# Kernel optimization log

Measured on AMD Instinct MI355X. Metric: run time of the kernel, lower is better.

## Reference

```python
import jax, jax.numpy as jnp
import numpy as np

EPS = 1.1920929e-07  # torch F.rms_norm default eps for fp32
D, NH, NKV, HD = 1024, 16, 4, 64
MLP_MULT, L = 3, 6           # L = num_layers // 2 shared blocks
VS, HS, LS, ROPE_B = 50257, 4096, 30.0, 10000.0
B, S = 2, 2048


def rmsn(x):
    return x * jax.lax.rsqrt(jnp.mean(jnp.square(x), -1, keepdims=True) + EPS)


def rope_tables(s):
    f = 1.0 / ROPE_B ** (jnp.arange(0, HD, 2, dtype=jnp.float32) / HD)
    fr = jnp.outer(jnp.arange(s, dtype=jnp.float32), f)  # [s, HD/2]
    return jnp.cos(fr), jnp.sin(fr)


def rot(x, c, s):
    h = x.shape[-1] // 2
    x1, x2 = x[..., :h], x[..., h:]
    return jnp.concatenate([x1 * c + x2 * s, -x1 * s + x2 * c], -1)


def attn(x, Wq, Wk, Wv, Wo, qg, cos, sin):
    b, s, d = x.shape
    q = (x @ Wq.T).reshape(b, s, NH, HD).swapaxes(1, 2)    # [b,nh,s,hd]
    k = (x @ Wk.T).reshape(b, s, NKV, HD).swapaxes(1, 2)   # [b,nkv,s,hd]
    v = (x @ Wv.T).reshape(b, s, NKV, HD).swapaxes(1, 2)
    q, k = rmsn(q), rmsn(k)                                # QK RMSNorm (no weight)
    c, si = cos[None, None], sin[None, None]
    q, k = rot(q, c, si), rot(k, c, si)
    q = q * qg[None, :, None, None]                        # per-head gate
    g = NH // NKV
    qr = q.reshape(b, NKV, g, s, HD)
    scores = jnp.einsum('bkgqd,bksd->bkgqs', qr, k) / jnp.sqrt(jnp.float32(HD))
    mask = jnp.tril(jnp.ones((s, s), bool))
    scores = jnp.where(mask, scores, -jnp.inf)
    p = jax.nn.softmax(scores, -1)
    y = jnp.einsum('bkgqs,bksd->bkgqd', p, v).reshape(b, NH, s, HD)
    y = y.swapaxes(1, 2).reshape(b, s, d)
    return y @ Wo.T


def mlp(x, Wf, Wo2):
    return jnp.square(jax.nn.relu(x @ Wf.T)) @ Wo2.T       # ReLU^2 MLP


def block(x, x0, p, cos, sin):
    Wq, Wk, Wv, Wo, qg, a_sc, m_sc, rm, Wf, Wo2 = p
    x = rm[0] * x + rm[1] * x0                             # learned residual mix
    x = x + a_sc * attn(rmsn(x), Wq, Wk, Wv, Wo, qg, cos, sin)
    x = x + m_sc * mlp(rmsn(x), Wf, Wo2)
    return x


def setup_inputs() -> dict:
    key = jax.random.key(0)
    ks = jax.random.split(key, 16)
    sd = 0.02
    return {
        'ids': jax.random.randint(ks[0], (B, S), 0, VS, dtype=jnp.int32),
        'y': jax.random.randint(ks[1], (B, S), 0, VS, dtype=jnp.int32),
        'u_emb': jax.random.normal(ks[2], (VS, D // 2), jnp.float32) * 0.02,
        'b_emb': jax.random.normal(ks[3], (HS, D // 2), jnp.float32) * 0.01,
        'Wq': jax.random.normal(ks[4], (L, D, D), jnp.float32) * sd,
        'Wk': jax.random.normal(ks[5], (L, NKV * HD, D), jnp.float32) * sd,
        'Wv': jax.random.normal(ks[6], (L, NKV * HD, D), jnp.float32) * sd,
        'Wo': jax.random.normal(ks[7], (L, D, D), jnp.float32) * sd,
        'qg': jnp.ones((L, NH), jnp.float32),
        'a_scale': jnp.ones((L, D), jnp.float32),
        'm_scale': jnp.ones((L, D), jnp.float32),
        'rm': jnp.stack([jnp.full((L, D), 0.7, jnp.float32), jnp.full((L, D), 0.3, jnp.float32)], 1),
        'Wf': jax.random.normal(ks[8], (L, MLP_MULT * D, D), jnp.float32) * sd,
        'Wo2': jax.random.normal(ks[9], (L, D, MLP_MULT * D), jnp.float32) * sd,
        'sw': jnp.ones((L, D), jnp.float32),
    }


def reference(ids, y, u_emb, b_emb, Wq, Wk, Wv, Wo, qg, a_scale, m_scale, rm, Wf, Wo2, sw):
    b, s = ids.shape
    # BigramHash embedding: (prev_id*VS + id) % HS, computed mod-HS to stay in int32
    pi = jnp.pad(ids[:, :-1], ((0, 0), (1, 0)))
    bi = (((pi % HS) * (VS % HS)) % HS + ids % HS) % HS
    h = jnp.concatenate([u_emb[ids], b_emb[bi]], -1)       # [b,s,D]
    h = rmsn(h)
    cos, sin = rope_tables(s)
    h0, sk = h, []
    for i in range(L):                                     # encoder half
        p = (Wq[i], Wk[i], Wv[i], Wo[i], qg[i], a_scale[i], m_scale[i], rm[i], Wf[i], Wo2[i])
        h = block(h, h0, p, cos, sin)
        sk.append(h)
    for i in range(L):                                     # decoder half (reversed blocks, skips)
        h = h + sw[i] * sk[L - 1 - i]
        j = L - 1 - i
        p = (Wq[j], Wk[j], Wv[j], Wo[j], qg[j], a_scale[j], m_scale[j], rm[j], Wf[j], Wo2[j])
        h = block(h, h0, p, cos, sin)
    h = rmsn(h)
    # tied bigram-hash head: out_weight = [u_emb | zeros]  ->  only first D/2 dims matter
    lg = h.reshape(-1, D)[:, :D // 2] @ u_emb.T            # [b*s, VS]
    lg = LS * jnp.tanh(lg / LS)                            # logit softcap
    logp = jax.nn.log_softmax(lg.astype(jnp.float32), -1)
    yf = y.reshape(-1)
    loss = -jnp.mean(jnp.take_along_axis(logp, yf[:, None], 1)[:, 0])
    return loss
```

## Files before the change

### kernel.cpp

```cpp
#include <hip/hip_runtime.h>
#include <cstdint>
#include <cstddef>

constexpr int   Dm    = 1024;
constexpr int   NHn   = 16;
constexpr int   NKVn  = 4;
constexpr int   HDn   = 64;
constexpr int   Ln    = 6;
constexpr int   Sn    = 2048;
constexpr int   Bn    = 2;
constexpr int   ROWS  = Bn * Sn;
constexpr int   VSn   = 50257;
constexpr int   HSn   = 4096;
constexpr float EPSF  = 1.1920929e-07f;
constexpr int   VCHUNK = 4096;
constexpr int   VPAD   = 50304;
constexpr float LOG2E  = 1.44269504f;

#define DEV __device__ __forceinline__

typedef __attribute__((ext_vector_type(8))) short bf16x8;
typedef __attribute__((ext_vector_type(4))) float f32x4;
using ush = unsigned short;

DEV ush f2bf(float f) {
    unsigned int u = __float_as_uint(f);
    u = (u + 0x7fffu + ((u >> 16) & 1u)) >> 16;
    return (ush)u;
}

DEV float b2f(ush v) {
    return __uint_as_float(((unsigned int)v) << 16);
}

DEV f32x4 mfma16(bf16x8 a, bf16x8 b, f32x4 c) {
    return __builtin_amdgcn_mfma_f32_16x16x32_bf16(a, b, c, 0, 0, 0);
}

DEV void llds16(const ush* g, ush* l) {
    __builtin_amdgcn_global_load_lds(
        (const __attribute__((address_space(1))) void*)g,
        (__attribute__((address_space(3))) void*)l, 16, 0, 0);
}

DEV float block_sum256(float v, float* red) {
#pragma unroll
    for (int off = 32; off; off >>= 1) v += __shfl_xor(v, off);
    __syncthreads();
    if ((threadIdx.x & 63) == 0) red[threadIdx.x >> 6] = v;
    __syncthreads();
    return red[0] + red[1] + red[2] + red[3];
}

DEV float block_max256(float v, float* red) {
#pragma unroll
    for (int off = 32; off; off >>= 1) v = fmaxf(v, __shfl_xor(v, off));
    __syncthreads();
    if ((threadIdx.x & 63) == 0) red[threadIdx.x >> 6] = v;
    __syncthreads();
    return fmaxf(fmaxf(red[0], red[1]), fmaxf(red[2], red[3]));
}

__global__ void rope_kernel(float* __restrict__ cb, float* __restrict__ sb) {
    int idx = blockIdx.x * 256 + threadIdx.x;
    if (idx >= Sn * 32) return;
    int t = idx >> 5, f = idx & 31;
    float freq = powf(10000.f, -(float)f * (1.f / 32.f));
    float ang  = (float)t * freq;
    cb[idx] = cosf(ang);
    sb[idx] = sinf(ang);
}

__global__ void cvt_bf16_kernel(const float* __restrict__ s, ush* __restrict__ d, int n4) {
    int i = blockIdx.x * 256 + threadIdx.x;
    if (i >= n4) return;
    float4 v = *(const float4*)(s + (size_t)i * 4);
    ushort4 o;
    o.x = f2bf(v.x); o.y = f2bf(v.y); o.z = f2bf(v.z); o.w = f2bf(v.w);
    *(ushort4*)(d + (size_t)i * 4) = o;
}

__global__ void zpad_kernel(ush* __restrict__ p, int n) {
    int i = blockIdx.x * 256 + threadIdx.x;
    if (i < n) p[i] = 0;
}

__global__ __launch_bounds__(256)
void embed_kernel(const int* __restrict__ ids, const float* __restrict__ ue,
                  const float* __restrict__ be, float* __restrict__ h,
                  float* __restrict__ h0) {
    __shared__ float red[4];
    int r = blockIdx.x;
    int s = r % Sn;
    int id = ids[r];
    int prev = (s == 0) ? 0 : ids[r - 1];
    int bi = ((prev % HSn) * (VSn % HSn) % HSn + id % HSn) % HSn;
    int tid = threadIdx.x;
    float vals[4];
    float ss = 0.f;
#pragma unroll
    for (int t = 0; t < 4; ++t) {
        int j = tid + t * 256;
        float v = (j < 512) ? ue[(size_t)id * 512 + j]
                            : be[(size_t)bi * 512 + (j - 512)];
        vals[t] = v; ss += v * v;
    }
    ss = block_sum256(ss, red);
    float rinv = rsqrtf(ss * (1.f / Dm) + EPSF);
#pragma unroll
    for (int t = 0; t < 4; ++t) {
        int j = tid + t * 256;
        float v = vals[t] * rinv;
        h [(size_t)r * Dm + j] = v;
        h0[(size_t)r * Dm + j] = v;
    }
}

__global__ __launch_bounds__(256)
void resmix_kernel(float* __restrict__ h, const float* __restrict__ h0,
                   const float* __restrict__ rm0, ush* __restrict__ xnb) {
    __shared__ float red[4];
    int r = blockIdx.x, tid = threadIdx.x;
    const float* rm1 = rm0 + Dm;
    float vals[4]; float ss = 0.f;
#pragma unroll
    for (int t = 0; t < 4; ++t) {
        int j = tid + t * 256;
        size_t o = (size_t)r * Dm + j;
        float v = rm0[j] * h[o] + rm1[j] * h0[o];
        vals[t] = v; ss += v * v;
        h[o] = v;
    }
    ss = block_sum256(ss, red);
    float rinv = rsqrtf(ss * (1.f / Dm) + EPSF);
#pragma unroll
    for (int t = 0; t < 4; ++t)
        xnb[(size_t)r * Dm + tid + t * 256] = f2bf(vals[t] * rinv);
}

__global__ __launch_bounds__(256)
void rmsn_kernel(const float* __restrict__ x, ush* __restrict__ out) {
    __shared__ float red[4];
    int r = blockIdx.x, tid = threadIdx.x;
    float vals[4]; float ss = 0.f;
#pragma unroll
    for (int t = 0; t < 4; ++t) {
        float v = x[(size_t)r * Dm + tid + t * 256];
        vals[t] = v; ss += v * v;
    }
    ss = block_sum256(ss, red);
    float rinv = rsqrtf(ss * (1.f / Dm) + EPSF);
#pragma unroll
    for (int t = 0; t < 4; ++t)
        out[(size_t)r * Dm + tid + t * 256] = f2bf(vals[t] * rinv);
}

__global__ __launch_bounds__(256)
void skipadd_kernel(float* __restrict__ h, const ush* __restrict__ skb,
                    const float* __restrict__ sc) {
    int r = blockIdx.x, tid = threadIdx.x;
#pragma unroll
    for (int t = 0; t < 4; ++t) {
        int j = tid + t * 256;
        size_t o = (size_t)r * Dm + j;
        h[o] = fmaf(sc[j], b2f(skb[o]), h[o]);
    }
}

template<int TM, int MODE>
__global__ __launch_bounds__(256)
void gemm_k(const ush* __restrict__ A, const ush* __restrict__ B,
            ush* __restrict__ C, int M, int N, int K,
            int lda, int ldb, int ldc,
            float* __restrict__ hres, const float* __restrict__ sc,
            ush* __restrict__ dup) {
    __shared__ __align__(16) ush As[TM * 32];
    __shared__ __align__(16) ush Bs[128 * 32];
    const int m0 = blockIdx.x * TM, n0 = blockIdx.y * 128;
    const int tid  = threadIdx.x;
    const int w    = tid >> 6, lane = tid & 63;
    const int l15  = lane & 15, quad = lane >> 4;
    const int wr   = w >> 1, wc = w & 1;
    constexpr int NI = TM / 32;

    const int srow = lane >> 2, sch = lane & 3;
    const ush* Ag;
    ush* AsW;
    if constexpr (TM == 128) {
        Ag  = A + (size_t)(m0 + w * 32 + srow) * lda + sch * 8;
        AsW = As + w * 1024;
    } else {
        Ag  = A + (size_t)(m0 + w * 16 + srow) * lda + sch * 8;
        AsW = As + w * 512;
    }
    const ush* Bg = B + (size_t)(n0 + w * 32 + srow) * ldb + sch * 8;
    ush* BsW = Bs + w * 1024;

    f32x4 acc[NI][4] = {};

    for (int k0 = 0; k0 < K; k0 += 32) {
        __syncthreads();
        llds16(Ag + k0, AsW);
        if constexpr (TM == 128) llds16(Ag + k0 + 16 * lda, AsW + 512);
        llds16(Bg + k0,            BsW);
        llds16(Bg + k0 + 16 * ldb, BsW + 512);
        __syncthreads();
        bf16x8 af[NI], bfv[4];
#pragma unroll
        for (int i = 0; i < NI; ++i)
            af[i] = *(const bf16x8*)&As[(wr * (TM / 2) + i * 16 + l15) * 32 + quad * 8];
#pragma unroll
        for (int j = 0; j < 4; ++j)
            bfv[j] = *(const bf16x8*)&Bs[(wc * 64 + j * 16 + l15) * 32 + quad * 8];
#pragma unroll
        for (int i = 0; i < NI; ++i)
#pragma unroll
            for (int j = 0; j < 4; ++j)
                acc[i][j] = mfma16(af[i], bfv[j], acc[i][j]);
    }

#pragma unroll
    for (int i = 0; i < NI; ++i) {
#pragma unroll
        for (int j = 0; j < 4; ++j) {
            int row = m0 + wr * (TM / 2) + i * 16 + quad * 4;
            int col = n0 + wc * 64 + j * 16 + l15;
#pragma unroll
            for (int r = 0; r < 4; ++r) {
                float v = acc[i][j][r];
                if (MODE == 1) { v = fmaxf(v, 0.f); v = v * v; }
                else if (MODE == 2) {
                    float ax = fabsf(v) * (1.f / 30.f);
                    float e  = __expf(-2.f * ax);
                    float t  = (1.f - e) / (1.f + e);
                    v = copysignf(t * 30.f, v);
                }
                if (MODE == 3) {
                    size_t o = (size_t)(row + r) * ldc + col;
                    float nv = fmaf(sc[col], v, hres[o]);
                    hres[o] = nv;
                    if (dup) dup[o] = f2bf(nv);
                } else {
                    C[(size_t)(row + r) * ldc + col] = f2bf(v);
                }
            }
        }
    }
}

__global__ __launch_bounds__(256)
void qknorm_rope_kernel(const ush* __restrict__ in, int in_ld, int in_off,
                        ush* __restrict__ out, int out_ld, int heads,
                        const float* __restrict__ cosb, const float* __restrict__ sinb,
                        const float* __restrict__ qg, float scale) {
    int row  = blockIdx.x * 4 + (threadIdx.x >> 6);
    int lane = threadIdx.x & 63;
    int hh   = row % heads;
    int t    = row / heads;
    int sidx = t % Sn;
    float x = b2f(in[(size_t)t * in_ld + in_off + hh * 64 + lane]);
    float ss = x * x;
#pragma unroll
    for (int off = 32; off; off >>= 1) ss += __shfl_xor(ss, off);
    float xn = x * rsqrtf(ss * (1.f / HDn) + EPSF);
    float partner = __shfl_xor(xn, 32);
    int f = lane & 31;
    float c  = cosb[sidx * 32 + f];
    float sv = sinb[sidx * 32 + f];
    float o = (lane < 32) ? fmaf(xn, c, partner * sv)
                          : fmaf(xn, c, -partner * sv);
    if (qg) o *= qg[hh] * scale;
    out[(size_t)t * out_ld + hh * 64 + lane] = f2bf(o);
}

__global__ __launch_bounds__(256)
void vtrans_kernel(const ush* __restrict__ in, int in_ld, int in_off,
                   ush* __restrict__ out) {
    __shared__ ush tile[32][33];
    int s0 = blockIdx.x * 32;
    int c0 = blockIdx.y * 32;
    int i = threadIdx.x >> 5;
    int j = threadIdx.x & 31;
#pragma unroll
    for (int k = 0; k < 4; ++k)
        tile[i + k * 8][j] = in[(size_t)(s0 + i + k * 8) * in_ld + in_off + c0 + j];
    __syncthreads();
#pragma unroll
    for (int k = 0; k < 4; ++k)
        out[(size_t)(c0 + i + k * 8) * (size_t)ROWS + s0 + j] = tile[j][i + k * 8];
}

__global__ __launch_bounds__(256)
void attn_mfma_kernel(const ush* __restrict__ qb,
                      const ush* __restrict__ kb,
                      const ush* __restrict__ vt,
                      ush* __restrict__ ob,
                      const float* __restrict__ qgl) {
    __shared__ __align__(16) ush Ks[64 * 72];
    __shared__ __align__(16) ush Vs[64 * 72];
    __shared__ __align__(16) ush Ps[64 * 72];
    const int tile = blockIdx.x & 31;
    const int h    = (blockIdx.x >> 5) & 15;
    const int b    = blockIdx.x >> 9;
    const int kvh  = h >> 2;
    const int w    = threadIdx.x >> 6, lane = threadIdx.x & 63;
    const int l15  = lane & 15, quad = lane >> 4;
    const int q0   = tile * 64;
    const float mfix = 8.f * fabsf(qgl[h]) * LOG2E;

    const size_t qrow = (size_t)(b * Sn + q0 + w * 16 + l15) * 1024 + h * 64;
    bf16x8 qf0 = *(const bf16x8*)(qb + qrow + quad * 8);
    bf16x8 qf1 = *(const bf16x8*)(qb + qrow + 32 + quad * 8);

    f32x4 Oacc[4] = {};
    float lsum[4] = {0.f, 0.f, 0.f, 0.f};
    const int qbase = q0 + w * 16 + quad * 4;

    const int nblk = tile + 1;
    for (int kb_i = 0; kb_i < nblk; ++kb_i) {
        const int k0 = kb_i * 64;
        __syncthreads();
        {
            const size_t kgb = (size_t)(b * Sn + k0) * 256 + kvh * 64;
            const size_t vgb = (size_t)(kvh * 64) * (size_t)ROWS + b * Sn + k0;
#pragma unroll
            for (int ii = 0; ii < 2; ++ii) {
                int idx = threadIdx.x + ii * 256;
                int rr = idx >> 3, ch = idx & 7;
                uint4 kvl = *(const uint4*)(kb + kgb + (size_t)rr * 256 + ch * 8);
                *(uint4*)&Ks[rr * 72 + ch * 8] = kvl;
                uint4 vvl = *(const uint4*)(vt + vgb + (size_t)rr * (size_t)ROWS + ch * 8);
                *(uint4*)&Vs[rr * 72 + ch * 8] = vvl;
            }
        }
        __syncthreads();

        f32x4 S[4] = {};
#pragma unroll
        for (int c = 0; c < 4; ++c) {
            bf16x8 kf0 = *(const bf16x8*)&Ks[(c * 16 + l15) * 72 + quad * 8];
            bf16x8 kf1 = *(const bf16x8*)&Ks[(c * 16 + l15) * 72 + 32 + quad * 8];
            S[c] = mfma16(qf0, kf0, S[c]);
            S[c] = mfma16(qf1, kf1, S[c]);
        }

        if (kb_i == tile) {
#pragma unroll
            for (int c = 0; c < 4; ++c) {
                int key = k0 + c * 16 + l15;
#pragma unroll
                for (int r = 0; r < 4; ++r)
                    if (key > qbase + r) S[c][r] = -INFINITY;
            }
        }
#pragma unroll
        for (int c = 0; c < 4; ++c)
#pragma unroll
            for (int r = 0; r < 4; ++r) {
                float p = exp2f(S[c][r] - mfix);
                S[c][r] = p;
                lsum[r] += p;
            }

#pragma unroll
        for (int c = 0; c < 4; ++c)
#pragma unroll
            for (int r = 0; r < 4; ++r)
                Ps[(w * 16 + quad * 4 + r) * 72 + c * 16 + l15] = f2bf(S[c][r]);

        bf16x8 pf0 = *(const bf16x8*)&Ps[(w * 16 + l15) * 72 + quad * 8];
        bf16x8 pf1 = *(const bf16x8*)&Ps[(w * 16 + l15) * 72 + 32 + quad * 8];
#pragma unroll
        for (int dt = 0; dt < 4; ++dt) {
            bf16x8 vf0 = *(const bf16x8*)&Vs[(dt * 16 + l15) * 72 + quad * 8];
            bf16x8 vf1 = *(const bf16x8*)&Vs[(dt * 16 + l15) * 72 + 32 + quad * 8];
            Oacc[dt] = mfma16(pf0, vf0, Oacc[dt]);
            Oacc[dt] = mfma16(pf1, vf1, Oacc[dt]);
        }
    }

#pragma unroll
    for (int m = 1; m <= 8; m <<= 1)
#pragma unroll
        for (int r = 0; r < 4; ++r)
            lsum[r] += __shfl_xor(lsum[r], m);

#pragma unroll
    for (int dt = 0; dt < 4; ++dt)
#pragma unroll
        for (int r = 0; r < 4; ++r) {
            size_t o = (size_t)(b * Sn + qbase + r) * 1024 + h * 64 + dt * 16 + l15;
            ob[o] = f2bf(Oacc[dt][r] / fmaxf(lsum[r], 1e-35f));
        }
}

__global__ void loss_init_kernel(float* __restrict__ m, float* __restrict__ s,
                                 float* __restrict__ tg) {
    int i = blockIdx.x * 256 + threadIdx.x;
    if (i < ROWS) { m[i] = -INFINITY; s[i] = 0.f; tg[i] = 0.f; }
}

__global__ __launch_bounds__(256)
void chunk_reduce_kernel(const ush* __restrict__ Cc, int Nc, int c0,
                         const int* __restrict__ y, float* __restrict__ m,
                         float* __restrict__ s, float* __restrict__ tg) {
    __shared__ float red[4];
    int r = blockIdx.x, tid = threadIdx.x;
    const ush* row = Cc + (size_t)r * VCHUNK;
    float v[16];
    float mx = -INFINITY;
#pragma unroll
    for (int t = 0; t < 16; ++t) {
        int j = tid + t * 256;
        v[t] = (j < Nc) ? b2f(row[j]) : -INFINITY;
        mx = fmaxf(mx, v[t]);
    }
    mx = block_max256(mx, red);
    float se = 0.f;
#pragma unroll
    for (int t = 0; t < 16; ++t)
        se += __expf(v[t] - mx);
    se = block_sum256(se, red);
    if (tid == 0) {
        float mo = m[r];
        float mn = fmaxf(mo, mx);
        s[r] = s[r] * __expf(mo - mn) + se * __expf(mx - mn);
        m[r] = mn;
        int t = y[r] - c0;
        if (t >= 0 && t < Nc) tg[r] = b2f(row[t]);
    }
}

__global__ __launch_bounds__(256)
void loss_final_kernel(const float* __restrict__ m, const float* __restrict__ s,
                       const float* __restrict__ tg, float* __restrict__ out) {
    __shared__ float red[4];
    float part = 0.f;
    for (int r = threadIdx.x; r < ROWS; r += 256)
        part += m[r] + logf(s[r]) - tg[r];
    part = block_sum256(part, red);
    if (threadIdx.x == 0) out[0] = part * (1.f / ROWS);
}

extern "C" void kernel_launch(void* const* d_in, const int* in_sizes, int n_in,
                              void* d_out, int out_size, void* d_ws, size_t ws_size,
                              hipStream_t stream) {
    const int*   ids = (const int*)d_in[0];
    const int*   yv  = (const int*)d_in[1];
    const float* ue  = (const float*)d_in[2];
    const float* be  = (const float*)d_in[3];
    const float* Wq  = (const float*)d_in[4];
    const float* Wk  = (const float*)d_in[5];
    const float* Wv  = (const float*)d_in[6];
    const float* Wo  = (const float*)d_in[7];
    const float* qg  = (const float*)d_in[8];
    const float* asc = (const float*)d_in[9];
    const float* msc = (const float*)d_in[10];
    const float* rm  = (const float*)d_in[11];
    const float* Wf  = (const float*)d_in[12];
    const float* Wo2 = (const float*)d_in[13];
    const float* sw  = (const float*)d_in[14];
    (void)in_sizes; (void)n_in; (void)out_size; (void)ws_size;

    char* wsb = (char*)d_ws;
    size_t off = 0;
    auto alloc = [&](size_t bytes) {
        void* p = (void*)(wsb + off);
        off += ((bytes + 255) & ~size_t(255));
        return p;
    };
    float* h    = (float*)alloc((size_t)ROWS * Dm * 4);
    float* h0   = (float*)alloc((size_t)ROWS * Dm * 4);
    float* cosb = (float*)alloc((size_t)Sn * 32 * 4);
    float* sinb = (float*)alloc((size_t)Sn * 32 * 4);
    float* mrow = (float*)alloc(ROWS * 4);
    float* srow = (float*)alloc(ROWS * 4);
    float* tgv  = (float*)alloc(ROWS * 4);
    ush* skb  = (ush*)alloc((size_t)Ln * ROWS * Dm * 2);
    ush* xnb  = (ush*)alloc((size_t)ROWS * Dm * 2);
    ush* qkvb = (ush*)alloc((size_t)ROWS * 1536 * 2);
    ush* qbf  = (ush*)alloc((size_t)ROWS * Dm * 2);
    ush* kbf  = (ush*)alloc((size_t)ROWS * 256 * 2);
    ush* vtb  = (ush*)alloc((size_t)256 * ROWS * 2);
    ush* attb = (ush*)alloc((size_t)ROWS * Dm * 2);
    ush* hidb = (ush*)alloc((size_t)ROWS * 3 * Dm * 2);
    ush* wbuf = (ush*)alloc((size_t)8704 * 1024 * 2);
    ush* ueb  = (ush*)alloc((size_t)VPAD * 512 * 2);
    ush* chunk = skb;

    ush* wqkvb = wbuf;
    ush* wob   = wbuf + (size_t)1536 * 1024;
    ush* wfb   = wbuf + (size_t)2560 * 1024;
    ush* wo2b  = wbuf + (size_t)5632 * 1024;

    auto cvt = [&](const float* s, ush* d, size_t n) {
        int n4 = (int)(n / 4);
        cvt_bf16_kernel<<<(n4 + 255) / 256, 256, 0, stream>>>(s, d, n4);
    };

    cvt(ue, ueb, (size_t)VSn * 512);
    zpad_kernel<<<((VPAD - VSn) * 512 + 255) / 256, 256, 0, stream>>>(
        ueb + (size_t)VSn * 512, (VPAD - VSn) * 512);

    rope_kernel<<<(Sn * 32 + 255) / 256, 256, 0, stream>>>(cosb, sinb);
    embed_kernel<<<ROWS, 256, 0, stream>>>(ids, ue, be, h, h0);

    auto run_block = [&](int l, ush* dup) {
        cvt(Wq + (size_t)l * Dm * Dm,       wqkvb,              (size_t)Dm * Dm);
        cvt(Wk + (size_t)l * 256 * Dm,      wqkvb + 1024 * Dm,  (size_t)256 * Dm);
        cvt(Wv + (size_t)l * 256 * Dm,      wqkvb + 1280 * Dm,  (size_t)256 * Dm);
        cvt(Wo + (size_t)l * Dm * Dm,       wob,                (size_t)Dm * Dm);
        cvt(Wf + (size_t)l * 3 * Dm * Dm,   wfb,                (size_t)3 * Dm * Dm);
        cvt(Wo2 + (size_t)l * 3 * Dm * Dm,  wo2b,               (size_t)3 * Dm * Dm);

        resmix_kernel<<<ROWS, 256, 0, stream>>>(h, h0, rm + (size_t)l * 2 * Dm, xnb);
        gemm_k<64, 0><<<dim3(ROWS / 64, 1536 / 128), 256, 0, stream>>>(
            xnb, wqkvb, qkvb, ROWS, 1536, Dm, Dm, Dm, 1536, nullptr, nullptr, nullptr);
        qknorm_rope_kernel<<<ROWS * NHn / 4, 256, 0, stream>>>(
            qkvb, 1536, 0, qbf, 1024, NHn, cosb, sinb,
            qg + (size_t)l * NHn, 0.125f * LOG2E);
        qknorm_rope_kernel<<<ROWS * NKVn / 4, 256, 0, stream>>>(
            qkvb, 1536, 1024, kbf, 256, NKVn, cosb, sinb, nullptr, 1.f);
        vtrans_kernel<<<dim3(ROWS / 32, 8), 256, 0, stream>>>(qkvb, 1536, 1280, vtb);
        attn_mfma_kernel<<<Bn * NHn * (Sn / 64), 256, 0, stream>>>(
            qbf, kbf, vtb, attb, qg + (size_t)l * NHn);
        gemm_k<64, 3><<<dim3(ROWS / 64, Dm / 128), 256, 0, stream>>>(
            attb, wob, nullptr, ROWS, Dm, Dm, Dm, Dm, Dm,
            h, asc + (size_t)l * Dm, nullptr);
        rmsn_kernel<<<ROWS, 256, 0, stream>>>(h, xnb);
        gemm_k<128, 1><<<dim3(ROWS / 128, 3 * Dm / 128), 256, 0, stream>>>(
            xnb, wfb, hidb, ROWS, 3 * Dm, Dm, Dm, Dm, 3 * Dm, nullptr, nullptr, nullptr);
        gemm_k<64, 3><<<dim3(ROWS / 64, Dm / 128), 256, 0, stream>>>(
            hidb, wo2b, nullptr, ROWS, Dm, 3 * Dm, 3 * Dm, 3 * Dm, Dm,
            h, msc + (size_t)l * Dm, dup);
    };

    for (int l = 0; l < Ln; ++l)
        run_block(l, skb + (size_t)l * ROWS * Dm);
    for (int i = 0; i < Ln; ++i) {
        int j = Ln - 1 - i;
        skipadd_kernel<<<ROWS, 256, 0, stream>>>(h, skb + (size_t)j * ROWS * Dm,
                                                 sw + (size_t)i * Dm);
        run_block(j, nullptr);
    }

    rmsn_kernel<<<ROWS, 256, 0, stream>>>(h, xnb);
    loss_init_kernel<<<(ROWS + 255) / 256, 256, 0, stream>>>(mrow, srow, tgv);
    for (int c0 = 0; c0 < VSn; c0 += VCHUNK) {
        int Nc = (VSn - c0 < VCHUNK) ? (VSn - c0) : VCHUNK;
        int Ng = (VPAD - c0 < VCHUNK) ? (VPAD - c0) : VCHUNK;
        gemm_k<128, 2><<<dim3(ROWS / 128, Ng / 128), 256, 0, stream>>>(
            xnb, ueb + (size_t)c0 * 512, chunk, ROWS, Ng, 512, Dm, 512, VCHUNK,
            nullptr, nullptr, nullptr);
        chunk_reduce_kernel<<<ROWS, 256, 0, stream>>>(chunk, Nc, c0, yv, mrow, srow, tgv);
    }
    loss_final_kernel<<<1, 256, 0, stream>>>(mrow, srow, tgv, (float*)d_out);
}
```

Before: 4.999 ms.

## Enlarge attention query tiles, prefetch K/V, merge qk-norm launches, hoist weight conversion

The attention kernel now processes 128 query rows per block, two 16-row fragments per wave, so each K/V tile loaded into shared memory is reused twice. It prefetches the next K/V tile into registers while computing, schedules heavy causal tiles first, and packs P as paired bf16 via perm. The Q and K norm/RoPE launches are merged into one kernel. Per-layer fp32-to-bf16 weight conversion is hoisted so all layers convert once up front instead of twice per forward (encoder and decoder reuse the same layers), at the cost of a larger weight buffer and more register pressure in attention.

```diff
diff --git a/kernel.cpp b/kernel.cpp
--- a/kernel.cpp
+++ b/kernel.cpp
@@ -249,16 +249,19 @@
 }
 
 __global__ __launch_bounds__(256)
-void qknorm_rope_kernel(const ush* __restrict__ in, int in_ld, int in_off,
-                        ush* __restrict__ out, int out_ld, int heads,
+void qknorm_rope_kernel(const ush* __restrict__ in,
+                        ush* __restrict__ qout, ush* __restrict__ kout,
                         const float* __restrict__ cosb, const float* __restrict__ sinb,
-                        const float* __restrict__ qg, float scale) {
-    int row  = blockIdx.x * 4 + (threadIdx.x >> 6);
+                        const float* __restrict__ qg) {
+    int idx  = blockIdx.x * 4 + (threadIdx.x >> 6);
     int lane = threadIdx.x & 63;
-    int hh   = row % heads;
-    int t    = row / heads;
+    int t, hh, in_off;
+    ush* outp; int out_ld;
+    bool isq = idx < ROWS * NHn;
+    if (isq) { t = idx >> 4; hh = idx & 15; in_off = hh * 64; outp = qout; out_ld = 1024; }
+    else { int i2 = idx - ROWS * NHn; t = i2 >> 2; hh = i2 & 3; in_off = 1024 + hh * 64; outp = kout; out_ld = 256; }
     int sidx = t % Sn;
-    float x = b2f(in[(size_t)t * in_ld + in_off + hh * 64 + lane]);
+    float x = b2f(in[(size_t)t * 1536 + in_off + lane]);
     float ss = x * x;
 #pragma unroll
     for (int off = 32; off; off >>= 1) ss += __shfl_xor(ss, off);
@@ -269,13 +272,12 @@
     float sv = sinb[sidx * 32 + f];
     float o = (lane < 32) ? fmaf(xn, c, partner * sv)
                           : fmaf(xn, c, -partner * sv);
-    if (qg) o *= qg[hh] * scale;
-    out[(size_t)t * out_ld + hh * 64 + lane] = f2bf(o);
-}
-
-__global__ __launch_bounds__(256)
-void vtrans_kernel(const ush* __restrict__ in, int in_ld, int in_off,
-                   ush* __restrict__ out) {
+    if (isq) o *= qg[hh] * (0.125f * LOG2E);
+    outp[(size_t)t * out_ld + hh * 64 + lane] = f2bf(o);
+}
+
+__global__ __launch_bounds__(256)
+void vtrans_kernel(const ush* __restrict__ in, ush* __restrict__ out) {
     __shared__ ush tile[32][33];
     int s0 = blockIdx.x * 32;
     int c0 = blockIdx.y * 32;
@@ -283,7 +285,7 @@
     int j = threadIdx.x & 31;
 #pragma unroll
     for (int k = 0; k < 4; ++k)
-        tile[i + k * 8][j] = in[(size_t)(s0 + i + k * 8) * in_ld + in_off + c0 + j];
+        tile[i + k * 8][j] = in[(size_t)(s0 + i + k * 8) * 1536 + 1280 + c0 + j];
     __syncthreads();
 #pragma unroll
     for (int k = 0; k < 4; ++k)
@@ -298,100 +300,137 @@
                       const float* __restrict__ qgl) {
     __shared__ __align__(16) ush Ks[64 * 72];
     __shared__ __align__(16) ush Vs[64 * 72];
-    __shared__ __align__(16) ush Ps[64 * 72];
-    const int tile = blockIdx.x & 31;
-    const int h    = (blockIdx.x >> 5) & 15;
-    const int b    = blockIdx.x >> 9;
+    __shared__ __align__(16) unsigned int PsD[128 * 36];
+    const int tile = 15 - (blockIdx.x & 15);
+    const int h    = (blockIdx.x >> 4) & 15;
+    const int b    = blockIdx.x >> 8;
     const int kvh  = h >> 2;
     const int w    = threadIdx.x >> 6, lane = threadIdx.x & 63;
     const int l15  = lane & 15, quad = lane >> 4;
-    const int q0   = tile * 64;
+    const int q0   = tile * 128;
     const float mfix = 8.f * fabsf(qgl[h]) * LOG2E;
 
-    const size_t qrow = (size_t)(b * Sn + q0 + w * 16 + l15) * 1024 + h * 64;
-    bf16x8 qf0 = *(const bf16x8*)(qb + qrow + quad * 8);
-    bf16x8 qf1 = *(const bf16x8*)(qb + qrow + 32 + quad * 8);
-
-    f32x4 Oacc[4] = {};
-    float lsum[4] = {0.f, 0.f, 0.f, 0.f};
-    const int qbase = q0 + w * 16 + quad * 4;
-
-    const int nblk = tile + 1;
+    bf16x8 qf[2][2];
+    {
+        size_t qr = (size_t)(b * Sn + q0 + w * 32 + l15) * 1024 + h * 64;
+        qf[0][0] = *(const bf16x8*)(qb + qr + quad * 8);
+        qf[0][1] = *(const bf16x8*)(qb + qr + 32 + quad * 8);
+        qf[1][0] = *(const bf16x8*)(qb + qr + 16 * 1024 + quad * 8);
+        qf[1][1] = *(const bf16x8*)(qb + qr + 16 * 1024 + 32 + quad * 8);
+    }
+    f32x4 Oacc[2][4] = {};
+    float lsum[2][4] = {{0.f,0.f,0.f,0.f},{0.f,0.f,0.f,0.f}};
+
+    const int rrS = threadIdx.x >> 3, chS = threadIdx.x & 7;
+    const size_t kbase = (size_t)(b * Sn) * 256 + kvh * 64;
+    const size_t vbase = (size_t)(kvh * 64) * (size_t)ROWS + b * Sn;
+    const int nblk = 2 * tile + 2;
+
+    uint4 kr0 = *(const uint4*)(kb + kbase + (size_t)rrS * 256 + chS * 8);
+    uint4 kr1 = *(const uint4*)(kb + kbase + (size_t)(rrS + 32) * 256 + chS * 8);
+    uint4 vr0 = *(const uint4*)(vt + vbase + (size_t)rrS * ROWS + chS * 8);
+    uint4 vr1 = *(const uint4*)(vt + vbase + (size_t)(rrS + 32) * ROWS + chS * 8);
+
     for (int kb_i = 0; kb_i < nblk; ++kb_i) {
         const int k0 = kb_i * 64;
         __syncthreads();
-        {
-            const size_t kgb = (size_t)(b * Sn + k0) * 256 + kvh * 64;
-            const size_t vgb = (size_t)(kvh * 64) * (size_t)ROWS + b * Sn + k0;
-#pragma unroll
-            for (int ii = 0; ii < 2; ++ii) {
-                int idx = threadIdx.x + ii * 256;
-                int rr = idx >> 3, ch = idx & 7;
-                uint4 kvl = *(const uint4*)(kb + kgb + (size_t)rr * 256 + ch * 8);
-                *(uint4*)&Ks[rr * 72 + ch * 8] = kvl;
-                uint4 vvl = *(const uint4*)(vt + vgb + (size_t)rr * (size_t)ROWS + ch * 8);
-                *(uint4*)&Vs[rr * 72 + ch * 8] = vvl;
-            }
+        *(uint4*)&Ks[rrS * 72 + chS * 8]        = kr0;
+        *(uint4*)&Ks[(rrS + 32) * 72 + chS * 8] = kr1;
+        *(uint4*)&Vs[rrS * 72 + chS * 8]        = vr0;
+        *(uint4*)&Vs[(rrS + 32) * 72 + chS * 8] = vr1;
+        __syncthreads();
+        if (kb_i + 1 < nblk) {
+            int k0n = k0 + 64;
+            kr0 = *(const uint4*)(kb + kbase + (size_t)(k0n + rrS) * 256 + chS * 8);
+            kr1 = *(const uint4*)(kb + kbase + (size_t)(k0n + rrS + 32) * 256 + chS * 8);
+            vr0 = *(const uint4*)(vt + vbase + (size_t)rrS * ROWS + k0n + chS * 8);
+            vr1 = *(const uint4*)(vt + vbase + (size_t)(rrS + 32) * ROWS + k0n + chS * 8);
         }
-        __syncthreads();
-
-        f32x4 S[4] = {};
+
+        f32x4 S0[4] = {}, S1[4] = {};
 #pragma unroll
         for (int c = 0; c < 4; ++c) {
             bf16x8 kf0 = *(const bf16x8*)&Ks[(c * 16 + l15) * 72 + quad * 8];
             bf16x8 kf1 = *(const bf16x8*)&Ks[(c * 16 + l15) * 72 + 32 + quad * 8];
-            S[c] = mfma16(qf0, kf0, S[c]);
-            S[c] = mfma16(qf1, kf1, S[c]);
+            S0[c] = mfma16(qf[0][0], kf0, S0[c]);
+            S0[c] = mfma16(qf[0][1], kf1, S0[c]);
+            S1[c] = mfma16(qf[1][0], kf0, S1[c]);
+            S1[c] = mfma16(qf[1][1], kf1, S1[c]);
         }
 
-        if (kb_i == tile) {
-#pragma unroll
-            for (int c = 0; c < 4; ++c) {
-                int key = k0 + c * 16 + l15;
-#pragma unroll
-                for (int r = 0; r < 4; ++r)
-                    if (key > qbase + r) S[c][r] = -INFINITY;
+#pragma unroll
+        for (int f = 0; f < 2; ++f) {
+            f32x4* S = f ? S1 : S0;
+            const int qbF = q0 + w * 32 + f * 16;
+            if (k0 + 63 > qbF) {
+#pragma unroll
+                for (int c = 0; c < 4; ++c) {
+                    int key = k0 + c * 16 + l15;
+#pragma unroll
+                    for (int r = 0; r < 4; ++r)
+                        if (key > qbF + quad * 4 + r) S[c][r] = -INFINITY;
+                }
+            }
+#pragma unroll
+            for (int c = 0; c < 4; ++c)
+#pragma unroll
+                for (int r = 0; r < 4; ++r) {
+                    float p = exp2f(S[c][r] - mfix);
+                    S[c][r] = p;
+                    lsum[f][r] += p;
+                }
+            const int prow = w * 32 + f * 16 + quad * 4;
+#pragma unroll
+            for (int cp = 0; cp < 2; ++cp)
+#pragma unroll
+                for (int r = 0; r < 4; ++r) {
+                    unsigned int pk = __builtin_amdgcn_perm(
+                        __float_as_uint(S[cp + 2][r]), __float_as_uint(S[cp][r]),
+                        0x07060302u);
+                    PsD[(prow + r) * 36 + cp * 16 + l15] = pk;
+                }
+        }
+
+#pragma unroll
+        for (int f = 0; f < 2; ++f) {
+            const int prow = w * 32 + f * 16 + l15;
+            unsigned int d[8];
+            *(uint4*)&d[0] = *(const uint4*)&PsD[prow * 36 + quad * 8];
+            *(uint4*)&d[4] = *(const uint4*)&PsD[prow * 36 + quad * 8 + 4];
+            unsigned int lo[4], hi[4];
+#pragma unroll
+            for (int t = 0; t < 4; ++t) {
+                lo[t] = __builtin_amdgcn_perm(d[2 * t + 1], d[2 * t], 0x05040100u);
+                hi[t] = __builtin_amdgcn_perm(d[2 * t + 1], d[2 * t], 0x07060302u);
+            }
+            bf16x8 pf0 = *(const bf16x8*)lo;
+            bf16x8 pf1 = *(const bf16x8*)hi;
+#pragma unroll
+            for (int dt = 0; dt < 4; ++dt) {
+                bf16x8 vf0 = *(const bf16x8*)&Vs[(dt * 16 + l15) * 72 + quad * 8];
+                bf16x8 vf1 = *(const bf16x8*)&Vs[(dt * 16 + l15) * 72 + 32 + quad * 8];
+                Oacc[f][dt] = mfma16(pf0, vf0, Oacc[f][dt]);
+                Oacc[f][dt] = mfma16(pf1, vf1, Oacc[f][dt]);
             }
         }
-#pragma unroll
-        for (int c = 0; c < 4; ++c)
+    }
+
+#pragma unroll
+    for (int f = 0; f < 2; ++f) {
+#pragma unroll
+        for (int m = 1; m <= 8; m <<= 1)
+#pragma unroll
+            for (int r = 0; r < 4; ++r)
+                lsum[f][r] += __shfl_xor(lsum[f][r], m);
+#pragma unroll
+        for (int dt = 0; dt < 4; ++dt)
 #pragma unroll
             for (int r = 0; r < 4; ++r) {
-                float p = exp2f(S[c][r] - mfix);
-                S[c][r] = p;
-                lsum[r] += p;
+                size_t o = (size_t)(b * Sn + q0 + w * 32 + f * 16 + quad * 4 + r) * 1024
+                         + h * 64 + dt * 16 + l15;
+                ob[o] = f2bf(Oacc[f][dt][r] / lsum[f][r]);
             }
-
-#pragma unroll
-        for (int c = 0; c < 4; ++c)
-#pragma unroll
-            for (int r = 0; r < 4; ++r)
-                Ps[(w * 16 + quad * 4 + r) * 72 + c * 16 + l15] = f2bf(S[c][r]);
-
-        bf16x8 pf0 = *(const bf16x8*)&Ps[(w * 16 + l15) * 72 + quad * 8];
-        bf16x8 pf1 = *(const bf16x8*)&Ps[(w * 16 + l15) * 72 + 32 + quad * 8];
-#pragma unroll
-        for (int dt = 0; dt < 4; ++dt) {
-            bf16x8 vf0 = *(const bf16x8*)&Vs[(dt * 16 + l15) * 72 + quad * 8];
-            bf16x8 vf1 = *(const bf16x8*)&Vs[(dt * 16 + l15) * 72 + 32 + quad * 8];
-            Oacc[dt] = mfma16(pf0, vf0, Oacc[dt]);
-            Oacc[dt] = mfma16(pf1, vf1, Oacc[dt]);
-        }
-    }
-
-#pragma unroll
-    for (int m = 1; m <= 8; m <<= 1)
-#pragma unroll
-        for (int r = 0; r < 4; ++r)
-            lsum[r] += __shfl_xor(lsum[r], m);
-
-#pragma unroll
-    for (int dt = 0; dt < 4; ++dt)
-#pragma unroll
-        for (int r = 0; r < 4; ++r) {
-            size_t o = (size_t)(b * Sn + qbase + r) * 1024 + h * 64 + dt * 16 + l15;
-            ob[o] = f2bf(Oacc[dt][r] / fmaxf(lsum[r], 1e-35f));
-        }
+    }
 }
 
 __global__ void loss_init_kernel(float* __restrict__ m, float* __restrict__ s,
@@ -484,20 +523,24 @@
     ush* vtb  = (ush*)alloc((size_t)256 * ROWS * 2);
     ush* attb = (ush*)alloc((size_t)ROWS * Dm * 2);
     ush* hidb = (ush*)alloc((size_t)ROWS * 3 * Dm * 2);
-    ush* wbuf = (ush*)alloc((size_t)8704 * 1024 * 2);
+    ush* wall = (ush*)alloc((size_t)Ln * 8704 * 1024 * 2);
     ush* ueb  = (ush*)alloc((size_t)VPAD * 512 * 2);
     ush* chunk = skb;
-
-    ush* wqkvb = wbuf;
-    ush* wob   = wbuf + (size_t)1536 * 1024;
-    ush* wfb   = wbuf + (size_t)2560 * 1024;
-    ush* wo2b  = wbuf + (size_t)5632 * 1024;
 
     auto cvt = [&](const float* s, ush* d, size_t n) {
         int n4 = (int)(n / 4);
         cvt_bf16_kernel<<<(n4 + 255) / 256, 256, 0, stream>>>(s, d, n4);
     };
 
+    for (int l = 0; l < Ln; ++l) {
+        ush* wl = wall + (size_t)l * 8704 * 1024;
+        cvt(Wq + (size_t)l * Dm * Dm,      wl,              (size_t)Dm * Dm);
+        cvt(Wk + (size_t)l * 256 * Dm,     wl + 1024 * Dm,  (size_t)256 * Dm);
+        cvt(Wv + (size_t)l * 256 * Dm,     wl + 1280 * Dm,  (size_t)256 * Dm);
+        cvt(Wo + (size_t)l * Dm * Dm,      wl + 1536 * Dm,  (size_t)Dm * Dm);
+        cvt(Wf + (size_t)l * 3 * Dm * Dm,  wl + 2560 * Dm,  (size_t)3 * Dm * Dm);
+        cvt(Wo2 + (size_t)l * 3 * Dm * Dm, wl + 5632 * Dm,  (size_t)3 * Dm * Dm);
+    }
     cvt(ue, ueb, (size_t)VSn * 512);
     zpad_kernel<<<((VPAD - VSn) * 512 + 255) / 256, 256, 0, stream>>>(
         ueb + (size_t)VSn * 512, (VPAD - VSn) * 512);
@@ -506,23 +549,19 @@
     embed_kernel<<<ROWS, 256, 0, stream>>>(ids, ue, be, h, h0);
 
     auto run_block = [&](int l, ush* dup) {
-        cvt(Wq + (size_t)l * Dm * Dm,       wqkvb,              (size_t)Dm * Dm);
-        cvt(Wk + (size_t)l * 256 * Dm,      wqkvb + 1024 * Dm,  (size_t)256 * Dm);
-        cvt(Wv + (size_t)l * 256 * Dm,      wqkvb + 1280 * Dm,  (size_t)256 * Dm);
-        cvt(Wo + (size_t)l * Dm * Dm,       wob,                (size_t)Dm * Dm);
-        cvt(Wf + (size_t)l * 3 * Dm * Dm,   wfb,                (size_t)3 * Dm * Dm);
-        cvt(Wo2 + (size_t)l * 3 * Dm * Dm,  wo2b,               (size_t)3 * Dm * Dm);
+        ush* wl    = wall + (size_t)l * 8704 * 1024;
+        ush* wqkvb = wl;
+        ush* wob   = wl + (size_t)1536 * 1024;
+        ush* wfb   = wl + (size_t)2560 * 1024;
+        ush* wo2b  = wl + (size_t)5632 * 1024;
 
         resmix_kernel<<<ROWS, 256, 0, stream>>>(h, h0, rm + (size_t)l * 2 * Dm, xnb);
         gemm_k<64, 0><<<dim3(ROWS / 64, 1536 / 128), 256, 0, stream>>>(
             xnb, wqkvb, qkvb, ROWS, 1536, Dm, Dm, Dm, 1536, nullptr, nullptr, nullptr);
-        qknorm_rope_kernel<<<ROWS * NHn / 4, 256, 0, stream>>>(
-            qkvb, 1536, 0, qbf, 1024, NHn, cosb, sinb,
-            qg + (size_t)l * NHn, 0.125f * LOG2E);
-        qknorm_rope_kernel<<<ROWS * NKVn / 4, 256, 0, stream>>>(
-            qkvb, 1536, 1024, kbf, 256, NKVn, cosb, sinb, nullptr, 1.f);
-        vtrans_kernel<<<dim3(ROWS / 32, 8), 256, 0, stream>>>(qkvb, 1536, 1280, vtb);
-        attn_mfma_kernel<<<Bn * NHn * (Sn / 64), 256, 0, stream>>>(
+        qknorm_rope_kernel<<<ROWS * (NHn + NKVn) / 4, 256, 0, stream>>>(
+            qkvb, qbf, kbf, cosb, sinb, qg + (size_t)l * NHn);
+        vtrans_kernel<<<dim3(ROWS / 32, 8), 256, 0, stream>>>(qkvb, vtb);
+        attn_mfma_kernel<<<Bn * NHn * 16, 256, 0, stream>>>(
             qbf, kbf, vtb, attb, qg + (size_t)l * NHn);
         gemm_k<64, 3><<<dim3(ROWS / 64, Dm / 128), 256, 0, stream>>>(
             attb, wob, nullptr, ROWS, Dm, Dm, Dm, Dm, Dm,
```

Result: faster. 4.390 ms (-12.2%).
